# Kernel tuning notes

Measured on AMD Instinct MI355X. Metric: run time of the kernel, lower is better.

The kernel has to match this reference:

```python
import jax, jax.numpy as jnp
import numpy as np

B, S, HID, H = 4, 1024, 1024, 16
D = HID // H  # head_dim = 64


def setup_inputs() -> dict:
    key = jax.random.key(0)
    k1, k2, k3, k4, k5 = jax.random.split(key, 5)
    hidden_states = jax.random.normal(k1, (B, S, HID), dtype=jnp.float32)
    # llama-style rotary tables, broadcastable to [B, H, S, D]
    inv_freq = 1.0 / (10000.0 ** (jnp.arange(0, D, 2, dtype=jnp.float32) / D))
    t = jnp.arange(S, dtype=jnp.float32)
    freqs = jnp.outer(t, inv_freq)                  # [S, D/2]
    emb = jnp.concatenate([freqs, freqs], axis=-1)  # [S, D]
    cos = jnp.cos(emb)[None, None]                  # [1,1,S,D]
    sin = jnp.sin(emb)[None, None]
    # causal mask: True = masked out, shape [B,1,S,S]
    causal = jnp.triu(jnp.ones((S, S), dtype=bool), k=1)
    attention_mask = jnp.broadcast_to(causal[None, None], (B, 1, S, S))
    Wq = jax.random.normal(k2, (HID, HID), dtype=jnp.float32) * (HID ** -0.5)
    Wk = jax.random.normal(k3, (HID, HID), dtype=jnp.float32) * (HID ** -0.5)
    return {"hidden_states": hidden_states, "cos": cos, "sin": sin,
            "attention_mask": attention_mask, "Wq": Wq, "Wk": Wk}


def _rotate_half(x):
    x1, x2 = x[..., : x.shape[-1] // 2], x[..., x.shape[-1] // 2:]
    return jnp.concatenate([-x2, x1], axis=-1)


def reference(hidden_states, cos, sin, attention_mask, Wq, Wk):
    b, s, _ = hidden_states.shape
    # nn.Linear: x @ W.T ; reshape to [b, h, s, d]
    q = jnp.einsum('bsm,nm->bsn', hidden_states, Wq).reshape(b, s, H, D).transpose(0, 2, 1, 3)
    k = jnp.einsum('bsm,nm->bsn', hidden_states, Wk).reshape(b, s, H, D).transpose(0, 2, 1, 3)
    # RoPE: cos/sin [1,1,s,d] broadcast over batch and heads
    c, sn = cos[:, :, :s], sin[:, :, :s]
    q = q * c + _rotate_half(q) * sn
    k = k * c + _rotate_half(k) * sn
    # scaled QK^T: [b,h,s,s]
    scores = jnp.einsum('bhqd,bhkd->bhqk', q, k) / jnp.sqrt(jnp.float32(D))
    scores = jnp.where(attention_mask, jnp.finfo(scores.dtype).min, scores)
    attn = jax.nn.softmax(scores.astype(jnp.float32), axis=-1).astype(q.dtype)
    return attn
```

## Files before the change

### kernel.cpp

```cpp
#include <hip/hip_runtime.h>
#include <hip/hip_bf16.h>

#define H 16
#define S 1024
#define HIDDEN 1024
#define D 64

typedef __bf16 bf16_t;
typedef __bf16 bf16x8 __attribute__((ext_vector_type(8)));
typedef __bf16 bf16x4 __attribute__((ext_vector_type(4)));
typedef float f32x4 __attribute__((ext_vector_type(4)));

__device__ static inline void gld_lds16(const bf16_t* g, bf16_t* l) {
  __builtin_amdgcn_global_load_lds(
      (const __attribute__((address_space(1))) unsigned int*)g,
      (__attribute__((address_space(3))) unsigned int*)l, 16, 0, 0);
}

__global__ void cvt3_kernel(const float* __restrict__ a, int na4,
                            const float* __restrict__ b, int nb4,
                            const float* __restrict__ c, int nc4,
                            bf16_t* __restrict__ oa, bf16_t* __restrict__ ob,
                            bf16_t* __restrict__ oc) {
  int total = na4 + nb4 + nc4;
  for (int i = blockIdx.x * blockDim.x + threadIdx.x; i < total;
       i += gridDim.x * blockDim.x) {
    const float* src; bf16_t* dst; int j = i;
    if (j < na4)            { src = a; dst = oa; }
    else if (j < na4 + nb4) { j -= na4; src = b; dst = ob; }
    else                    { j -= na4 + nb4; src = c; dst = oc; }
    float4 v = ((const float4*)src)[j];
    bf16x4 o = { (bf16_t)v.x, (bf16_t)v.y, (bf16_t)v.z, (bf16_t)v.w };
    ((bf16x4*)dst)[j] = o;
  }
}

__global__ __launch_bounds__(256) void proj_rope_kernel(
    const bf16_t* __restrict__ hb,
    const bf16_t* __restrict__ wqb,
    const bf16_t* __restrict__ wkb,
    const float* __restrict__ cosp,
    const float* __restrict__ sinp,
    bf16_t* __restrict__ qout,
    bf16_t* __restrict__ kout) {
  __shared__ bf16_t As[128 * 32];
  __shared__ bf16_t Bs[128 * 32];
  const bf16_t* wb = (blockIdx.z == 0) ? wqb : wkb;
  bf16_t* outp     = (blockIdx.z == 0) ? qout : kout;
  int lane = threadIdx.x & 63;
  int w    = threadIdx.x >> 6;
  int c    = lane & 15;
  int quad = lane >> 4;
  int bm0 = blockIdx.x * 128;
  int bn0 = blockIdx.y * 128;
  int wm  = (w >> 1) * 64;
  int wn  = (w & 1) * 64;

  int slot0 = threadIdx.x;
  int slot1 = slot0 + 256;
  const bf16_t* gA0 = hb + (size_t)(bm0 + (slot0 >> 2)) * HIDDEN + (slot0 & 3) * 8;
  const bf16_t* gA1 = hb + (size_t)(bm0 + (slot1 >> 2)) * HIDDEN + (slot1 & 3) * 8;
  const bf16_t* gB0 = wb + (size_t)(bn0 + (slot0 >> 2)) * HIDDEN + (slot0 & 3) * 8;
  const bf16_t* gB1 = wb + (size_t)(bn0 + (slot1 >> 2)) * HIDDEN + (slot1 & 3) * 8;
  bf16_t* lA0 = As + w * 512;
  bf16_t* lA1 = As + 2048 + w * 512;
  bf16_t* lB0 = Bs + w * 512;
  bf16_t* lB1 = Bs + 2048 + w * 512;

  f32x4 acc[4][4] = {};
  for (int k0 = 0; k0 < HIDDEN; k0 += 32) {
    __syncthreads();
    gld_lds16(gA0 + k0, lA0);
    gld_lds16(gA1 + k0, lA1);
    gld_lds16(gB0 + k0, lB0);
    gld_lds16(gB1 + k0, lB1);
    __syncthreads();
    bf16x8 af[4], bfv[4];
#pragma unroll
    for (int i = 0; i < 4; i++)
      af[i] = *(const bf16x8*)(As + (wm + i * 16 + c) * 32 + quad * 8);
#pragma unroll
    for (int j = 0; j < 4; j++)
      bfv[j] = *(const bf16x8*)(Bs + (wn + j * 16 + c) * 32 + quad * 8);
#pragma unroll
    for (int i = 0; i < 4; i++)
#pragma unroll
      for (int j = 0; j < 4; j++)
        acc[i][j] = __builtin_amdgcn_mfma_f32_16x16x32_bf16(af[i], bfv[j], acc[i][j], 0, 0, 0);
  }

  int h = (bn0 + wn) >> 6;
#pragma unroll
  for (int j = 0; j < 4; j++) {
    int d = (wn + j * 16 + c) & 63;
#pragma unroll
    for (int i = 0; i < 4; i++) {
#pragma unroll
      for (int r = 0; r < 4; r++) {
        int srow = bm0 + wm + i * 16 + quad * 4 + r;
        int bb = srow >> 10;
        int sq = srow & (S - 1);
        float cth = cosp[sq * D + d];
        float sth = sinp[sq * D + d];
        float x = acc[i][j][r];
        float other = acc[i][j ^ 2][r];
        float rot = (j < 2) ? -other : other;
        outp[((size_t)(bb * H + h) * S + sq) * D + d] = (bf16_t)(x * cth + rot * sth);
      }
    }
  }
}

__global__ __launch_bounds__(256) void attn_kernel(
    const bf16_t* __restrict__ qb, const bf16_t* __restrict__ kb,
    float* __restrict__ out) {
  __shared__ float ssum[4][16];
  int lane = threadIdx.x & 63;
  int w    = threadIdx.x >> 6;
  int c    = lane & 15;
  int quad = lane >> 4;
  int bh = blockIdx.y;
  int q0 = blockIdx.x * 16;
  const bf16_t* Q = qb + (size_t)bh * S * D;
  const bf16_t* K = kb + (size_t)bh * S * D;
  int c0 = w * 256;
  int qmax = q0 + 15;
  int tlive = ((qmax - c0) >> 4) + 1;
  if (tlive < 0) tlive = 0;
  if (tlive > 16) tlive = 16;

  f32x4 acc[16] = {};
  bf16x8 a0 = *(const bf16x8*)(Q + (q0 + c) * D + quad * 8);
  bf16x8 a1 = *(const bf16x8*)(Q + (q0 + c) * D + quad * 8 + 32);
#pragma unroll
  for (int t = 0; t < 16; t++) {
    if (t < tlive) {
      int ct = c0 + t * 16;
      bf16x8 b0 = *(const bf16x8*)(K + (ct + c) * D + quad * 8);
      bf16x8 b1 = *(const bf16x8*)(K + (ct + c) * D + quad * 8 + 32);
      acc[t] = __builtin_amdgcn_mfma_f32_16x16x32_bf16(a0, b0, acc[t], 0, 0, 0);
      acc[t] = __builtin_amdgcn_mfma_f32_16x16x32_bf16(a1, b1, acc[t], 0, 0, 0);
    }
  }
  const float kSc = 0.125f * 1.44269504f;
  float sum[4] = {0.f, 0.f, 0.f, 0.f};
#pragma unroll
  for (int t = 0; t < 16; t++) {
    if (t < tlive) {
      int col = c0 + t * 16 + c;
#pragma unroll
      for (int r = 0; r < 4; r++) {
        int row = q0 + quad * 4 + r;
        float p = __builtin_amdgcn_exp2f(acc[t][r] * kSc);
        if (col > row) p = 0.0f;
        acc[t][r] = p;
        sum[r] += p;
      }
    }
  }
#pragma unroll
  for (int off = 1; off < 16; off <<= 1) {
#pragma unroll
    for (int r = 0; r < 4; r++) sum[r] += __shfl_xor(sum[r], off, 64);
  }
  if (c == 0) {
#pragma unroll
    for (int r = 0; r < 4; r++) ssum[w][quad * 4 + r] = sum[r];
  }
  __syncthreads();
  float inv[4];
#pragma unroll
  for (int r = 0; r < 4; r++) {
    int row = quad * 4 + r;
    inv[r] = __builtin_amdgcn_rcpf(ssum[0][row] + ssum[1][row] +
                                   ssum[2][row] + ssum[3][row]);
  }
#pragma unroll
  for (int t = 0; t < 16; t++) {
    int col = c0 + t * 16 + c;
#pragma unroll
    for (int r = 0; r < 4; r++) {
      int row = q0 + quad * 4 + r;
      float val = (t < tlive) ? acc[t][r] * inv[r] : 0.0f;
      out[((size_t)bh * S + row) * S + col] = val;
    }
  }
}

extern "C" void kernel_launch(void* const* d_in, const int* in_sizes, int n_in,
                              void* d_out, int out_size, void* d_ws, size_t ws_size,
                              hipStream_t stream) {
  const float* hidden = (const float*)d_in[0];
  const float* cosp   = (const float*)d_in[1];
  const float* sinp   = (const float*)d_in[2];
  const float* Wq = (const float*)d_in[4];
  const float* Wk = (const float*)d_in[5];
  float* out = (float*)d_out;

  char* ws = (char*)d_ws;
  bf16_t* hb   = (bf16_t*)(ws);
  bf16_t* wqb  = (bf16_t*)(ws + 8388608);
  bf16_t* wkb  = (bf16_t*)(ws + 10485760);
  bf16_t* qbuf = (bf16_t*)(ws + 12582912);
  bf16_t* kbuf = (bf16_t*)(ws + 20971520);

  int na4 = (4 * S * HIDDEN) / 4;
  int nb4 = (HIDDEN * HIDDEN) / 4;
  int total4 = na4 + nb4 + nb4;
  cvt3_kernel<<<dim3((total4 + 255) / 256), 256, 0, stream>>>(
      hidden, na4, Wq, nb4, Wk, nb4, hb, wqb, wkb);
  proj_rope_kernel<<<dim3(32, 8, 2), 256, 0, stream>>>(
      hb, wqb, wkb, cosp, sinp, qbuf, kbuf);
  attn_kernel<<<dim3(64, 64), 256, 0, stream>>>(qbuf, kbuf, out);
}
```

Measured before the change: 355.3 us.

## Double-buffer swizzled GEMM tiles and transpose attention MFMA for vectorized stores

The projection GEMM now uses a 64-wide K tile, double-buffered in LDS with an XOR swizzle. This overlaps global-to-LDS loads with MFMA work and avoids bank conflicts. The attention kernel swaps the MFMA operands so each lane holds four consecutive key columns of one query row. Output can then be written as 16-byte nontemporal float4 stores instead of scattered scalar stores, and the row-sum reduction needs fewer shuffles. K loads are also batched in groups of four to give more memory-level parallelism. The costs are doubled LDS use per block, which may lower occupancy, and more registers held in flight.

Result: slower. 364.0 us (+2.5%).

```diff
diff --git a/kernel.cpp b/kernel.cpp
--- a/kernel.cpp
+++ b/kernel.cpp
@@ -43,8 +43,8 @@
     const float* __restrict__ sinp,
     bf16_t* __restrict__ qout,
     bf16_t* __restrict__ kout) {
-  __shared__ bf16_t As[128 * 32];
-  __shared__ bf16_t Bs[128 * 32];
+  __shared__ bf16_t As[2][128 * 64];
+  __shared__ bf16_t Bs[2][128 * 64];
   const bf16_t* wb = (blockIdx.z == 0) ? wqb : wkb;
   bf16_t* outp     = (blockIdx.z == 0) ? qout : kout;
   int lane = threadIdx.x & 63;
@@ -56,37 +56,56 @@
   int wm  = (w >> 1) * 64;
   int wn  = (w & 1) * 64;
 
-  int slot0 = threadIdx.x;
-  int slot1 = slot0 + 256;
-  const bf16_t* gA0 = hb + (size_t)(bm0 + (slot0 >> 2)) * HIDDEN + (slot0 & 3) * 8;
-  const bf16_t* gA1 = hb + (size_t)(bm0 + (slot1 >> 2)) * HIDDEN + (slot1 & 3) * 8;
-  const bf16_t* gB0 = wb + (size_t)(bn0 + (slot0 >> 2)) * HIDDEN + (slot0 & 3) * 8;
-  const bf16_t* gB1 = wb + (size_t)(bn0 + (slot1 >> 2)) * HIDDEN + (slot1 & 3) * 8;
-  bf16_t* lA0 = As + w * 512;
-  bf16_t* lA1 = As + 2048 + w * 512;
-  bf16_t* lB0 = Bs + w * 512;
-  bf16_t* lB1 = Bs + 2048 + w * 512;
+  const bf16_t* gA[4]; const bf16_t* gB[4]; int loff[4];
+#pragma unroll
+  for (int i = 0; i < 4; i++) {
+    int s   = threadIdx.x + i * 256;
+    int row = s >> 3;
+    int cg  = (s & 7) ^ (row & 7);
+    gA[i]   = hb + (size_t)(bm0 + row) * HIDDEN + cg * 8;
+    gB[i]   = wb + (size_t)(bn0 + row) * HIDDEN + cg * 8;
+    loff[i] = (i * 256 + w * 64) * 8;
+  }
 
   f32x4 acc[4][4] = {};
-  for (int k0 = 0; k0 < HIDDEN; k0 += 32) {
+
+#pragma unroll
+  for (int i = 0; i < 4; i++) gld_lds16(gA[i], &As[0][loff[i]]);
+#pragma unroll
+  for (int i = 0; i < 4; i++) gld_lds16(gB[i], &Bs[0][loff[i]]);
+  __syncthreads();
+
+  for (int t = 0; t < 16; t++) {
+    int cur = t & 1;
+    if (t < 15) {
+      int k0 = (t + 1) * 64;
+#pragma unroll
+      for (int i = 0; i < 4; i++) gld_lds16(gA[i] + k0, &As[cur ^ 1][loff[i]]);
+#pragma unroll
+      for (int i = 0; i < 4; i++) gld_lds16(gB[i] + k0, &Bs[cur ^ 1][loff[i]]);
+    }
+#pragma unroll
+    for (int kk = 0; kk < 2; kk++) {
+      bf16x8 af[4], bfv[4];
+#pragma unroll
+      for (int i = 0; i < 4; i++) {
+        int row = wm + i * 16 + c;
+        int cl  = ((kk << 2) | quad) ^ (c & 7);
+        af[i] = *(const bf16x8*)(&As[cur][row * 64 + cl * 8]);
+      }
+#pragma unroll
+      for (int j = 0; j < 4; j++) {
+        int row = wn + j * 16 + c;
+        int cl  = ((kk << 2) | quad) ^ (c & 7);
+        bfv[j] = *(const bf16x8*)(&Bs[cur][row * 64 + cl * 8]);
+      }
+#pragma unroll
+      for (int i = 0; i < 4; i++)
+#pragma unroll
+        for (int j = 0; j < 4; j++)
+          acc[i][j] = __builtin_amdgcn_mfma_f32_16x16x32_bf16(af[i], bfv[j], acc[i][j], 0, 0, 0);
+    }
     __syncthreads();
-    gld_lds16(gA0 + k0, lA0);
-    gld_lds16(gA1 + k0, lA1);
-    gld_lds16(gB0 + k0, lB0);
-    gld_lds16(gB1 + k0, lB1);
-    __syncthreads();
-    bf16x8 af[4], bfv[4];
-#pragma unroll
-    for (int i = 0; i < 4; i++)
-      af[i] = *(const bf16x8*)(As + (wm + i * 16 + c) * 32 + quad * 8);
-#pragma unroll
-    for (int j = 0; j < 4; j++)
-      bfv[j] = *(const bf16x8*)(Bs + (wn + j * 16 + c) * 32 + quad * 8);
-#pragma unroll
-    for (int i = 0; i < 4; i++)
-#pragma unroll
-      for (int j = 0; j < 4; j++)
-        acc[i][j] = __builtin_amdgcn_mfma_f32_16x16x32_bf16(af[i], bfv[j], acc[i][j], 0, 0, 0);
   }
 
   int h = (bn0 + wn) >> 6;
@@ -133,57 +152,59 @@
   bf16x8 a0 = *(const bf16x8*)(Q + (q0 + c) * D + quad * 8);
   bf16x8 a1 = *(const bf16x8*)(Q + (q0 + c) * D + quad * 8 + 32);
 #pragma unroll
+  for (int g = 0; g < 4; g++) {
+    bf16x8 k0v[4], k1v[4];
+#pragma unroll
+    for (int u = 0; u < 4; u++) {
+      int t = g * 4 + u;
+      if (t < tlive) {
+        int ct = c0 + t * 16;
+        k0v[u] = *(const bf16x8*)(K + (ct + c) * D + quad * 8);
+        k1v[u] = *(const bf16x8*)(K + (ct + c) * D + quad * 8 + 32);
+      }
+    }
+#pragma unroll
+    for (int u = 0; u < 4; u++) {
+      int t = g * 4 + u;
+      if (t < tlive) {
+        acc[t] = __builtin_amdgcn_mfma_f32_16x16x32_bf16(k0v[u], a0, acc[t], 0, 0, 0);
+        acc[t] = __builtin_amdgcn_mfma_f32_16x16x32_bf16(k1v[u], a1, acc[t], 0, 0, 0);
+      }
+    }
+  }
+  const float kSc = 0.125f * 1.44269504f;
+  int qrow = q0 + c;
+  float sum = 0.f;
+#pragma unroll
   for (int t = 0; t < 16; t++) {
     if (t < tlive) {
-      int ct = c0 + t * 16;
-      bf16x8 b0 = *(const bf16x8*)(K + (ct + c) * D + quad * 8);
-      bf16x8 b1 = *(const bf16x8*)(K + (ct + c) * D + quad * 8 + 32);
-      acc[t] = __builtin_amdgcn_mfma_f32_16x16x32_bf16(a0, b0, acc[t], 0, 0, 0);
-      acc[t] = __builtin_amdgcn_mfma_f32_16x16x32_bf16(a1, b1, acc[t], 0, 0, 0);
-    }
-  }
-  const float kSc = 0.125f * 1.44269504f;
-  float sum[4] = {0.f, 0.f, 0.f, 0.f};
+      int kbase = c0 + t * 16 + quad * 4;
+#pragma unroll
+      for (int r = 0; r < 4; r++) {
+        float p = __builtin_amdgcn_exp2f(acc[t][r] * kSc);
+        if (kbase + r > qrow) p = 0.0f;
+        acc[t][r] = p;
+        sum += p;
+      }
+    }
+  }
+  sum += __shfl_xor(sum, 16, 64);
+  sum += __shfl_xor(sum, 32, 64);
+  if (quad == 0) ssum[w][c] = sum;
+  __syncthreads();
+  float inv = __builtin_amdgcn_rcpf(ssum[0][c] + ssum[1][c] +
+                                    ssum[2][c] + ssum[3][c]);
+  float* orow = out + ((size_t)bh * S + qrow) * S + c0 + quad * 4;
 #pragma unroll
   for (int t = 0; t < 16; t++) {
+    f32x4 v;
     if (t < tlive) {
-      int col = c0 + t * 16 + c;
-#pragma unroll
-      for (int r = 0; r < 4; r++) {
-        int row = q0 + quad * 4 + r;
-        float p = __builtin_amdgcn_exp2f(acc[t][r] * kSc);
-        if (col > row) p = 0.0f;
-        acc[t][r] = p;
-        sum[r] += p;
-      }
-    }
-  }
-#pragma unroll
-  for (int off = 1; off < 16; off <<= 1) {
-#pragma unroll
-    for (int r = 0; r < 4; r++) sum[r] += __shfl_xor(sum[r], off, 64);
-  }
-  if (c == 0) {
-#pragma unroll
-    for (int r = 0; r < 4; r++) ssum[w][quad * 4 + r] = sum[r];
-  }
-  __syncthreads();
-  float inv[4];
-#pragma unroll
-  for (int r = 0; r < 4; r++) {
-    int row = quad * 4 + r;
-    inv[r] = __builtin_amdgcn_rcpf(ssum[0][row] + ssum[1][row] +
-                                   ssum[2][row] + ssum[3][row]);
-  }
-#pragma unroll
-  for (int t = 0; t < 16; t++) {
-    int col = c0 + t * 16 + c;
-#pragma unroll
-    for (int r = 0; r < 4; r++) {
-      int row = q0 + quad * 4 + r;
-      float val = (t < tlive) ? acc[t][r] * inv[r] : 0.0f;
-      out[((size_t)bh * S + row) * S + col] = val;
-    }
+#pragma unroll
+      for (int r = 0; r < 4; r++) v[r] = acc[t][r] * inv;
+    } else {
+      v = (f32x4){0.f, 0.f, 0.f, 0.f};
+    }
+    __builtin_nontemporal_store(v, (f32x4*)(orow + t * 16));
   }
 }
 
```
